# Kernel tuning notes

Measured on AMD Instinct MI355X. Metric: run time of the kernel, lower is better.

The kernel has to match this reference:

```python
import jax, jax.numpy as jnp
import numpy as np


def setup_inputs() -> dict:
    key = jax.random.key(0)
    k1, k2 = jax.random.split(key)
    B, D, NUM_CLASSES = 8192, 128, 100
    features = jax.random.normal(k1, (B, D), dtype=jnp.float32)
    labels = jax.random.randint(k2, (B,), 0, NUM_CLASSES, dtype=jnp.int64)
    return {"features": features, "labels": labels}


def reference(features, labels):
    # temperature=0.07, clamp(min=0.01) -> 0.07
    TEMP = 0.07
    B = features.shape[0]
    dt = features.dtype

    # positive mask from labels: [B, B]
    mask = (labels[:, None] == labels[None, :]).astype(dt)

    # L2 normalize rows (F.normalize: x / max(||x||, eps))
    norm = jnp.sqrt(jnp.sum(features * features, axis=1, keepdims=True))
    f = features / jnp.maximum(norm, 1e-8)

    # similarity matrix, scaled and clamped to [-10, 10]
    sim = jnp.clip(jnp.matmul(f, f.T) / TEMP, -10.0, 10.0)

    eye = jnp.eye(B, dtype=dt)
    exp_sim = jnp.exp(sim)

    pos_sum = jnp.maximum(jnp.sum(exp_sim * (mask - eye), axis=1), 1e-8)
    neg_sum = jnp.maximum(jnp.sum(exp_sim * (1.0 - eye), axis=1), 1e-8)

    loss = -jnp.log(pos_sum / neg_sum)
    # NaN guard as in the original (returns 0 if any NaN)
    return jnp.where(jnp.any(jnp.isnan(loss)), jnp.zeros((), dt), jnp.mean(loss))
```

## Files before the change

### kernel.cpp

```cpp
#include <hip/hip_runtime.h>
#include <hip/hip_bf16.h>


using floatx4 = __attribute__((ext_vector_type(4))) float;
using intx4   = __attribute__((ext_vector_type(4))) int;
using intx8   = __attribute__((ext_vector_type(8))) int;
using llong2  = __attribute__((ext_vector_type(2))) long long;

constexpr int   Bn = 8192;
constexpr int   Dk = 128;
constexpr int   NSLICE = 32;
constexpr int   NBLK   = 32 * 32;
constexpr float PRESCALE = 4.5398160f;
constexpr float CLAMP    = 14.4269504f;
constexpr float LN2      = 0.69314718056f;
constexpr int   SCALE1   = 0x7F7F7F7F;

__global__ __launch_bounds__(256) void normalize_k(
    const float* __restrict__ feat, unsigned char* __restrict__ fb,
    float* __restrict__ rowpos, float* __restrict__ rowneg,
    unsigned int* __restrict__ done) {
  if (blockIdx.x < 32) {
    rowpos[blockIdx.x * 256 + threadIdx.x] = 0.f;
    rowneg[blockIdx.x * 256 + threadIdx.x] = 0.f;
  }
  if (blockIdx.x == 32 && threadIdx.x == 0) *done = 0u;
  const int row  = blockIdx.x * 4 + (threadIdx.x >> 6);
  const int lane = threadIdx.x & 63;
  const float2 v = ((const float2*)(feat + (size_t)row * Dk))[lane];
  float s = v.x * v.x + v.y * v.y;
#pragma unroll
  for (int m = 1; m < 64; m <<= 1) s += __shfl_xor(s, m);
  const float inv = PRESCALE / fmaxf(sqrtf(s), 1e-8f);
  const int packed = __builtin_amdgcn_cvt_pk_fp8_f32(v.x * inv, v.y * inv, 0, false);
  const int k0 = 2 * lane;
  const int p  = ((k0 & 31) >> 3) * 32 + (k0 >> 5) * 8 + (k0 & 7);
  *(unsigned short*)(fb + (size_t)row * Dk + p) = (unsigned short)(packed & 0xffff);
}

__global__ __launch_bounds__(256, 2) void simloss_k(
    const unsigned char* __restrict__ fb, const int* __restrict__ labels,
    float* __restrict__ rowpos, float* __restrict__ rowneg,
    unsigned int* __restrict__ done, float* __restrict__ out) {
  __shared__ __align__(16) unsigned char Bsh[256 * Dk];

  const int t     = threadIdx.x;
  const int lane  = t & 63;
  const int wave  = t >> 6;
  const int quad  = lane >> 4;
  const int lr    = lane & 15;
  const int jbase = blockIdx.x * 256;

  {
    const int chunk = t & 7;
    const int r0    = t >> 3;
#pragma unroll
    for (int it = 0; it < 8; ++it) {
      const int row = r0 + it * 32;
      const llong2 v = *(const llong2*)(fb + (size_t)(jbase + row) * Dk + chunk * 16);
      *(llong2*)(Bsh + row * Dk + ((chunk ^ (row & 7)) * 16)) = v;
    }
  }

  int labj16[8];
#pragma unroll
  for (int j = 0; j < 8; ++j) {
    const int l0 = labels[jbase + (2 * j) * 16 + lr];
    const int l1 = labels[jbase + (2 * j + 1) * 16 + lr];
    labj16[j] = l0 | (l1 << 16);
  }

  bool dl[4];
#pragma unroll
  for (int r = 0; r < 4; ++r) dl[r] = (quad * 4 + r) == lr;

  const int sw  = lr & 7;
  const int ch0 = ((quad * 2)     ^ sw) * 16;
  const int ch1 = ((quad * 2 + 1) ^ sw) * 16;

  __syncthreads();

#pragma unroll 1
  for (int p = 0; p < 2; ++p) {
    const int ibase = blockIdx.y * 256 + wave * 64 + p * 32;

    intx8 A0, A1;
    {
      const unsigned char* ap0 = fb + (size_t)(ibase + lr) * Dk + quad * 32;
      A0 = *(const intx8*)(ap0);
      A1 = *(const intx8*)(ap0 + 16 * Dk);
    }

    int li[2][4];
#pragma unroll
    for (int tt = 0; tt < 2; ++tt)
#pragma unroll
      for (int r = 0; r < 4; ++r)
        li[tt][r] = labels[ibase + tt * 16 + quad * 4 + r];

    float pos[2][4] = {};
    float neg[2][4] = {};

#pragma unroll
    for (int jt = 0; jt < 16; ++jt) {
      const unsigned char* bp = Bsh + (jt * 16 + lr) * Dk;
      const intx4 Blo = *(const intx4*)(bp + ch0);
      const intx4 Bhi = *(const intx4*)(bp + ch1);
      intx8 Bv;
      Bv[0] = Blo[0]; Bv[1] = Blo[1]; Bv[2] = Blo[2]; Bv[3] = Blo[3];
      Bv[4] = Bhi[0]; Bv[5] = Bhi[1]; Bv[6] = Bhi[2]; Bv[7] = Bhi[3];

      floatx4 acc0 = {0.f, 0.f, 0.f, 0.f};
      floatx4 acc1 = {0.f, 0.f, 0.f, 0.f};
      acc0 = __builtin_amdgcn_mfma_scale_f32_16x16x128_f8f6f4(
          A0, Bv, acc0, 0, 0, 0, SCALE1, 0, SCALE1);
      acc1 = __builtin_amdgcn_mfma_scale_f32_16x16x128_f8f6f4(
          A1, Bv, acc1, 0, 0, 0, SCALE1, 0, SCALE1);

      const int j0 = jbase + jt * 16;
      const int lj = (jt & 1) ? (labj16[jt >> 1] >> 16) : (labj16[jt >> 1] & 0xffff);
      float e0, e1, e2, e3;
      e0 = __builtin_amdgcn_exp2f(__builtin_amdgcn_fmed3f(acc0[0], -CLAMP, CLAMP));
      e1 = __builtin_amdgcn_exp2f(__builtin_amdgcn_fmed3f(acc0[1], -CLAMP, CLAMP));
      e2 = __builtin_amdgcn_exp2f(__builtin_amdgcn_fmed3f(acc0[2], -CLAMP, CLAMP));
      e3 = __builtin_amdgcn_exp2f(__builtin_amdgcn_fmed3f(acc0[3], -CLAMP, CLAMP));
      if (j0 == ibase) {
        if (dl[0]) e0 = 0.f;
        if (dl[1]) e1 = 0.f;
        if (dl[2]) e2 = 0.f;
        if (dl[3]) e3 = 0.f;
      }
      neg[0][0] += e0; neg[0][1] += e1; neg[0][2] += e2; neg[0][3] += e3;
      pos[0][0] += (li[0][0] == lj) ? e0 : 0.f;
      pos[0][1] += (li[0][1] == lj) ? e1 : 0.f;
      pos[0][2] += (li[0][2] == lj) ? e2 : 0.f;
      pos[0][3] += (li[0][3] == lj) ? e3 : 0.f;
      e0 = __builtin_amdgcn_exp2f(__builtin_amdgcn_fmed3f(acc1[0], -CLAMP, CLAMP));
      e1 = __builtin_amdgcn_exp2f(__builtin_amdgcn_fmed3f(acc1[1], -CLAMP, CLAMP));
      e2 = __builtin_amdgcn_exp2f(__builtin_amdgcn_fmed3f(acc1[2], -CLAMP, CLAMP));
      e3 = __builtin_amdgcn_exp2f(__builtin_amdgcn_fmed3f(acc1[3], -CLAMP, CLAMP));
      if (j0 == ibase + 16) {
        if (dl[0]) e0 = 0.f;
        if (dl[1]) e1 = 0.f;
        if (dl[2]) e2 = 0.f;
        if (dl[3]) e3 = 0.f;
      }
      neg[1][0] += e0; neg[1][1] += e1; neg[1][2] += e2; neg[1][3] += e3;
      pos[1][0] += (li[1][0] == lj) ? e0 : 0.f;
      pos[1][1] += (li[1][1] == lj) ? e1 : 0.f;
      pos[1][2] += (li[1][2] == lj) ? e2 : 0.f;
      pos[1][3] += (li[1][3] == lj) ? e3 : 0.f;
    }

#pragma unroll
    for (int tt = 0; tt < 2; ++tt)
#pragma unroll
      for (int r = 0; r < 4; ++r) {
        float p2 = pos[tt][r], n2 = neg[tt][r];
#pragma unroll
        for (int m = 1; m < 16; m <<= 1) {
          p2 += __shfl_xor(p2, m);
          n2 += __shfl_xor(n2, m);
        }
        if (lr == 0) {
          const int row = ibase + tt * 16 + quad * 4 + r;
          atomicAdd(&rowpos[row], p2);
          atomicAdd(&rowneg[row], n2);
        }
      }

    __builtin_amdgcn_sched_barrier(0);
  }

  __syncthreads();
  int* flag = (int*)Bsh;
  if (t == 0) {
    __threadfence();
    const unsigned int old = atomicAdd(done, 1u);
    *flag = (old == (unsigned)(NBLK - 1)) ? 1 : 0;
  }
  __syncthreads();
  if (*flag) {
    __threadfence();
    float acc = 0.f;
#pragma unroll
    for (int r = 0; r < Bn / 256; ++r) {
      const int row = r * 256 + t;
      const float pp = fmaxf(rowpos[row], 1e-8f);
      const float nn = fmaxf(rowneg[row], 1e-8f);
      acc += __builtin_amdgcn_logf(nn) - __builtin_amdgcn_logf(pp);
    }
#pragma unroll
    for (int m = 1; m < 64; m <<= 1) acc += __shfl_xor(acc, m);
    float* red = (float*)Bsh + 16;
    if (lane == 0) red[wave] = acc;
    __syncthreads();
    if (t == 0)
      *out = (red[0] + red[1] + red[2] + red[3]) * (LN2 / (float)Bn);
  }
}

extern "C" void kernel_launch(void* const* d_in, const int* in_sizes, int n_in,
                              void* d_out, int out_size, void* d_ws, size_t ws_size,
                              hipStream_t stream) {
  const float* feat   = (const float*)d_in[0];
  const int*   labels = (const int*)d_in[1];
  float* out = (float*)d_out;

  unsigned char* fb = (unsigned char*)d_ws;
  float* rowpos = (float*)((char*)d_ws + (size_t)Bn * Dk);
  float* rowneg = rowpos + Bn;
  unsigned int* done = (unsigned int*)(rowneg + Bn);

  normalize_k<<<Bn / 4, 256, 0, stream>>>(feat, fb, rowpos, rowneg, done);
  dim3 grid(NSLICE, 32);
  simloss_k<<<grid, 256, 0, stream>>>(fb, labels, rowpos, rowneg, done, out);
}
```

Before: 96.58 us.

## Exploit similarity matrix symmetry by computing only upper-triangular tile blocks

Launches 528 blocks covering only the upper triangle of 256x256 tiles (bi<=bj) instead of the full 32x32 grid. Off-diagonal blocks also reduce column sums into shared memory and atomically add them to the transposed rows, since the similarity matrix is symmetric. This roughly halves the MFMA and exp work. In exchange it adds cross-lane shuffles and LDS accumulation per tile, plus extra atomics. The FP8 rounding is symmetric, so results stay consistent.

```diff
diff --git a/kernel.cpp b/kernel.cpp
--- a/kernel.cpp
+++ b/kernel.cpp
@@ -9,8 +9,7 @@
 
 constexpr int   Bn = 8192;
 constexpr int   Dk = 128;
-constexpr int   NSLICE = 32;
-constexpr int   NBLK   = 32 * 32;
+constexpr int   NBLK   = 528;
 constexpr float PRESCALE = 4.5398160f;
 constexpr float CLAMP    = 14.4269504f;
 constexpr float LN2      = 0.69314718056f;
@@ -43,13 +42,25 @@
     float* __restrict__ rowpos, float* __restrict__ rowneg,
     unsigned int* __restrict__ done, float* __restrict__ out) {
   __shared__ __align__(16) unsigned char Bsh[256 * Dk];
+  __shared__ float colsc[4][2][256];
 
   const int t     = threadIdx.x;
   const int lane  = t & 63;
   const int wave  = t >> 6;
   const int quad  = lane >> 4;
   const int lr    = lane & 15;
-  const int jbase = blockIdx.x * 256;
+
+  int kk = blockIdx.x, bi = 0, accb = 0;
+  while (accb + (32 - bi) <= kk) { accb += 32 - bi; ++bi; }
+  const int  bj   = bi + (kk - accb);
+  const bool diag = (bi == bj);
+  const int  jbase = bj * 256;
+
+  {
+    float* cz = &colsc[0][0][0];
+#pragma unroll
+    for (int z = 0; z < 8; ++z) cz[t + z * 256] = 0.f;
+  }
 
   {
     const int chunk = t & 7;
@@ -82,7 +93,7 @@
 
 #pragma unroll 1
   for (int p = 0; p < 2; ++p) {
-    const int ibase = blockIdx.y * 256 + wave * 64 + p * 32;
+    const int ibase = bi * 256 + wave * 64 + p * 32;
 
     intx8 A0, A1;
     {
@@ -119,37 +130,51 @@
 
       const int j0 = jbase + jt * 16;
       const int lj = (jt & 1) ? (labj16[jt >> 1] >> 16) : (labj16[jt >> 1] & 0xffff);
-      float e0, e1, e2, e3;
-      e0 = __builtin_amdgcn_exp2f(__builtin_amdgcn_fmed3f(acc0[0], -CLAMP, CLAMP));
-      e1 = __builtin_amdgcn_exp2f(__builtin_amdgcn_fmed3f(acc0[1], -CLAMP, CLAMP));
-      e2 = __builtin_amdgcn_exp2f(__builtin_amdgcn_fmed3f(acc0[2], -CLAMP, CLAMP));
-      e3 = __builtin_amdgcn_exp2f(__builtin_amdgcn_fmed3f(acc0[3], -CLAMP, CLAMP));
-      if (j0 == ibase) {
-        if (dl[0]) e0 = 0.f;
-        if (dl[1]) e1 = 0.f;
-        if (dl[2]) e2 = 0.f;
-        if (dl[3]) e3 = 0.f;
+      float e0 = __builtin_amdgcn_exp2f(__builtin_amdgcn_fmed3f(acc0[0], -CLAMP, CLAMP));
+      float e1 = __builtin_amdgcn_exp2f(__builtin_amdgcn_fmed3f(acc0[1], -CLAMP, CLAMP));
+      float e2 = __builtin_amdgcn_exp2f(__builtin_amdgcn_fmed3f(acc0[2], -CLAMP, CLAMP));
+      float e3 = __builtin_amdgcn_exp2f(__builtin_amdgcn_fmed3f(acc0[3], -CLAMP, CLAMP));
+      float f0 = __builtin_amdgcn_exp2f(__builtin_amdgcn_fmed3f(acc1[0], -CLAMP, CLAMP));
+      float f1 = __builtin_amdgcn_exp2f(__builtin_amdgcn_fmed3f(acc1[1], -CLAMP, CLAMP));
+      float f2 = __builtin_amdgcn_exp2f(__builtin_amdgcn_fmed3f(acc1[2], -CLAMP, CLAMP));
+      float f3 = __builtin_amdgcn_exp2f(__builtin_amdgcn_fmed3f(acc1[3], -CLAMP, CLAMP));
+      if (diag) {
+        if (j0 == ibase) {
+          if (dl[0]) e0 = 0.f;
+          if (dl[1]) e1 = 0.f;
+          if (dl[2]) e2 = 0.f;
+          if (dl[3]) e3 = 0.f;
+        }
+        if (j0 == ibase + 16) {
+          if (dl[0]) f0 = 0.f;
+          if (dl[1]) f1 = 0.f;
+          if (dl[2]) f2 = 0.f;
+          if (dl[3]) f3 = 0.f;
+        }
       }
+      const float m0 = (li[0][0] == lj) ? e0 : 0.f;
+      const float m1 = (li[0][1] == lj) ? e1 : 0.f;
+      const float m2 = (li[0][2] == lj) ? e2 : 0.f;
+      const float m3 = (li[0][3] == lj) ? e3 : 0.f;
+      const float n0 = (li[1][0] == lj) ? f0 : 0.f;
+      const float n1 = (li[1][1] == lj) ? f1 : 0.f;
+      const float n2 = (li[1][2] == lj) ? f2 : 0.f;
+      const float n3 = (li[1][3] == lj) ? f3 : 0.f;
       neg[0][0] += e0; neg[0][1] += e1; neg[0][2] += e2; neg[0][3] += e3;
-      pos[0][0] += (li[0][0] == lj) ? e0 : 0.f;
-      pos[0][1] += (li[0][1] == lj) ? e1 : 0.f;
-      pos[0][2] += (li[0][2] == lj) ? e2 : 0.f;
-      pos[0][3] += (li[0][3] == lj) ? e3 : 0.f;
-      e0 = __builtin_amdgcn_exp2f(__builtin_amdgcn_fmed3f(acc1[0], -CLAMP, CLAMP));
-      e1 = __builtin_amdgcn_exp2f(__builtin_amdgcn_fmed3f(acc1[1], -CLAMP, CLAMP));
-      e2 = __builtin_amdgcn_exp2f(__builtin_amdgcn_fmed3f(acc1[2], -CLAMP, CLAMP));
-      e3 = __builtin_amdgcn_exp2f(__builtin_amdgcn_fmed3f(acc1[3], -CLAMP, CLAMP));
-      if (j0 == ibase + 16) {
-        if (dl[0]) e0 = 0.f;
-        if (dl[1]) e1 = 0.f;
-        if (dl[2]) e2 = 0.f;
-        if (dl[3]) e3 = 0.f;
+      neg[1][0] += f0; neg[1][1] += f1; neg[1][2] += f2; neg[1][3] += f3;
+      pos[0][0] += m0; pos[0][1] += m1; pos[0][2] += m2; pos[0][3] += m3;
+      pos[1][0] += n0; pos[1][1] += n1; pos[1][2] += n2; pos[1][3] += n3;
+
+      if (!diag) {
+        float cn = ((e0 + e1) + (e2 + e3)) + ((f0 + f1) + (f2 + f3));
+        float cp = ((m0 + m1) + (m2 + m3)) + ((n0 + n1) + (n2 + n3));
+        cn += __shfl_xor(cn, 16); cn += __shfl_xor(cn, 32);
+        cp += __shfl_xor(cp, 16); cp += __shfl_xor(cp, 32);
+        if (quad == 0) {
+          colsc[wave][0][jt * 16 + lr] += cp;
+          colsc[wave][1][jt * 16 + lr] += cn;
+        }
       }
-      neg[1][0] += e0; neg[1][1] += e1; neg[1][2] += e2; neg[1][3] += e3;
-      pos[1][0] += (li[1][0] == lj) ? e0 : 0.f;
-      pos[1][1] += (li[1][1] == lj) ? e1 : 0.f;
-      pos[1][2] += (li[1][2] == lj) ? e2 : 0.f;
-      pos[1][3] += (li[1][3] == lj) ? e3 : 0.f;
     }
 
 #pragma unroll
@@ -170,6 +195,14 @@
       }
 
     __builtin_amdgcn_sched_barrier(0);
+  }
+
+  if (!diag) {
+    __syncthreads();
+    const float cp = colsc[0][0][t] + colsc[1][0][t] + colsc[2][0][t] + colsc[3][0][t];
+    const float cn = colsc[0][1][t] + colsc[1][1][t] + colsc[2][1][t] + colsc[3][1][t];
+    atomicAdd(&rowpos[jbase + t], cp);
+    atomicAdd(&rowneg[jbase + t], cn);
   }
 
   __syncthreads();
@@ -213,6 +246,5 @@
   unsigned int* done = (unsigned int*)(rowneg + Bn);
 
   normalize_k<<<Bn / 4, 256, 0, stream>>>(feat, fb, rowpos, rowneg, done);
-  dim3 grid(NSLICE, 32);
-  simloss_k<<<grid, 256, 0, stream>>>(fb, labels, rowpos, rowneg, done, out);
+  simloss_k<<<NBLK, 256, 0, stream>>>(fb, labels, rowpos, rowneg, done, out);
 }
```

After: 153.3 us. 58.7% more time.
